# Kernel optimization log

Measured on AMD Instinct MI355X. Metric: run time of the kernel, lower is better.

The kernel has to match this reference:

```python
import jax, jax.numpy as jnp
import numpy as np

NODE_DIM, HIDDEN, PROJ = 5, 128, 256
NUM_MP = 3
BOX = 1.0


def _knn_edges(positions, k, box_length=BOX):
    """Periodic kNN graph. positions: (B,N,3) -> (src, dst) global flat indices, E = B*N*k."""
    B, N, _ = positions.shape

    def per_batch(pos):  # (N,3)
        delta = jnp.abs(pos[:, None, :] - pos[None, :, :])          # (N,N,3)
        delta = jnp.where(delta > 0.5 * box_length, box_length - delta, delta)
        dist = jnp.sqrt(jnp.sum(delta * delta, axis=-1) + 1e-12)    # (N,N)
        _, idx = jax.lax.top_k(-dist, k + 1)                        # k+1 smallest
        return idx[:, 1:]                                           # drop self -> (N,k)

    nbrs = jax.vmap(per_batch)(positions)                           # (B,N,k)
    offset = (jnp.arange(B) * N)[:, None, None]
    src = jnp.broadcast_to(jnp.arange(N)[None, :, None], (B, N, k)) + offset
    dst = nbrs + offset
    return src.reshape(-1), dst.reshape(-1)


def setup_inputs() -> dict:
    key = jax.random.key(0)
    ks = jax.random.split(key, 16)
    B, N = 8, 2048
    s = 0.05
    inp = {
        "x": jax.random.normal(ks[0], (B, N, NODE_DIM), jnp.float32),
        "positions": jax.random.uniform(ks[1], (B, N, 3), jnp.float32),
        "k": 16,
        # encoder: Linear(5,128)+ReLU, Linear(128,128)+ReLU
        "enc_w0": jax.random.normal(ks[2], (NODE_DIM, HIDDEN), jnp.float32) * s,
        "enc_b0": jnp.zeros((HIDDEN,), jnp.float32),
        "enc_w1": jax.random.normal(ks[3], (HIDDEN, HIDDEN), jnp.float32) * s,
        "enc_b1": jnp.zeros((HIDDEN,), jnp.float32),
        # message nets: Linear(2H,H)+ReLU per round
        "msg_w": jax.random.normal(ks[4], (NUM_MP, 2 * HIDDEN, HIDDEN), jnp.float32) * s,
        "msg_b": jnp.zeros((NUM_MP, HIDDEN), jnp.float32),
        # update nets: Linear(2H,H)+ReLU per round
        "upd_w": jax.random.normal(ks[5], (NUM_MP, 2 * HIDDEN, HIDDEN), jnp.float32) * s,
        "upd_b": jnp.zeros((NUM_MP, HIDDEN), jnp.float32),
        # projection head: Linear(H,H)+ReLU, Linear(H,proj)
        "proj_w0": jax.random.normal(ks[6], (HIDDEN, HIDDEN), jnp.float32) * s,
        "proj_b0": jnp.zeros((HIDDEN,), jnp.float32),
        "proj_w1": jax.random.normal(ks[7], (HIDDEN, PROJ), jnp.float32) * s,
        "proj_b1": jnp.zeros((PROJ,), jnp.float32),
    }
    return inp


def reference(x, positions, k, enc_w0, enc_b0, enc_w1, enc_b1,
              msg_w, msg_b, upd_w, upd_b, proj_w0, proj_b0, proj_w1, proj_b1):
    B, N, _ = x.shape
    BN = B * N
    relu = jax.nn.relu

    # encoder over flattened nodes
    h = relu(x.reshape(BN, -1) @ enc_w0 + enc_b0)
    h = relu(h @ enc_w1 + enc_b1)

    src, dst = _knn_edges(positions, k)
    E = src.shape[0]
    deg = jax.ops.segment_sum(jnp.ones((E,), h.dtype), dst, num_segments=BN)
    inv_deg = 1.0 / jnp.clip(deg, 1.0)

    for i in range(NUM_MP):
        # per-edge message: concat(sender, receiver) -> Linear+ReLU
        msg = relu(jnp.concatenate([h[src], h[dst]], axis=-1) @ msg_w[i] + msg_b[i])
        # mean aggregation at destination nodes
        agg = jax.ops.segment_sum(msg, dst, num_segments=BN) * inv_deg[:, None]
        # residual update
        h = h + relu(jnp.concatenate([h, agg], axis=-1) @ upd_w[i] + upd_b[i])

    z = relu(h @ proj_w0 + proj_b0) @ proj_w1 + proj_b1
    return z.reshape(B, N, PROJ), h.reshape(B, N, HIDDEN)
```

## Files before the change

### kernel.cpp

```cpp
#include <hip/hip_runtime.h>
#include <stdint.h>
#include <math.h>

#define NN 2048
#define BB 8
#define BN (BB*NN)
#define KK 16
#define EE (BN*KK)
#define HID 128
#define PROJ_D 256
#define QPB 16

typedef unsigned long long u64;
typedef unsigned short ushort_t;
typedef __attribute__((ext_vector_type(8))) short short8;
typedef __attribute__((ext_vector_type(4))) float f32x4;

__device__ __forceinline__ u64 wave_min_u64(u64 v) {
  #pragma unroll
  for (int off = 32; off > 0; off >>= 1) {
    u64 o = __shfl_xor(v, off);
    v = o < v ? o : v;
  }
  return v;
}

__global__ __launch_bounds__(1024) void knn_kernel(const float* __restrict__ pos,
                                                   int* __restrict__ nbr,
                                                   int* __restrict__ cnt) {
  __shared__ float4 Ps[NN];
  __shared__ unsigned Hist[QPB * 256];
  const int b  = blockIdx.x >> 7;
  const int qb = blockIdx.x & 127;
  const int wave = threadIdx.x >> 6;
  const int lane = threadIdx.x & 63;
  const int i = qb * QPB + wave;
  const float* P = pos + (size_t)b * NN * 3;

  for (int t = threadIdx.x; t < NN; t += 1024)
    Ps[t] = make_float4(P[t*3], P[t*3+1], P[t*3+2], 0.f);
  __syncthreads();

  const float4 pi = Ps[i];
  const float xi = pi.x, yi = pi.y, zi = pi.z;
  unsigned* H = &Hist[wave * 256];

  float d[32];
  #pragma unroll
  for (int t = 0; t < 32; t++) {
    int j = t * 64 + lane;
    float4 pj = Ps[j];
    float ax = fabsf(xi - pj.x), ay = fabsf(yi - pj.y), az = fabsf(zi - pj.z);
    float dx = fminf(ax, 1.0f - ax);
    float dy = fminf(ay, 1.0f - ay);
    float dz = fminf(az, 1.0f - az);
    float s = __fadd_rn(__fadd_rn(__fadd_rn(__fmul_rn(dx,dx), __fmul_rn(dy,dy)),
                                  __fmul_rn(dz,dz)), 1e-12f);
    d[t] = __fsqrt_rn(s);
  }

  float scale = 1024.0f;
  int bstar = 0; unsigned C = 0;
  for (;;) {
    *(uint4*)&H[lane * 4] = make_uint4(0u, 0u, 0u, 0u);
    #pragma unroll
    for (int t = 0; t < 32; t++) {
      int bin = (int)(d[t] * scale);
      if (bin < 256) atomicAdd(&H[bin], 1u);
    }
    uint4 cv = *(const uint4*)&H[lane * 4];
    unsigned s4 = cv.x + cv.y + cv.z + cv.w;
    unsigned incl = s4;
    #pragma unroll
    for (int off = 1; off < 64; off <<= 1) {
      unsigned v = __shfl_up(incl, off);
      if (lane >= off) incl += v;
    }
    unsigned total = __shfl(incl, 63);
    if (total >= 17u) {
      unsigned base = incl - s4;
      bool has = (incl >= 17u) && (base < 17u);
      u64 hmask = __ballot(has);
      int srcl = __ffsll((unsigned long long)hmask) - 1;
      int bl = 0; unsigned Cl = 0;
      if (has) {
        if (base + cv.x >= 17u)                    { bl = lane*4 + 0; Cl = base; }
        else if (base + cv.x + cv.y >= 17u)        { bl = lane*4 + 1; Cl = base + cv.x; }
        else if (base + cv.x + cv.y + cv.z >= 17u) { bl = lane*4 + 2; Cl = base + cv.x + cv.y; }
        else                                       { bl = lane*4 + 3; Cl = base + cv.x + cv.y + cv.z; }
      }
      bstar = __shfl(bl, srcl);
      C     = __shfl(Cl, srcl);
      break;
    }
    scale *= 0.25f;
  }
  const int m = 17 - (int)C;

  u64 lst[6];
  #pragma unroll
  for (int t = 0; t < 6; t++) lst[t] = ~0ull;
  #pragma unroll
  for (int t = 0; t < 32; t++) {
    int bin = (int)(d[t] * scale);
    u64 key = ((u64)__float_as_uint(d[t]) << 11) | (unsigned)(t * 64 + lane);
    u64 cand = (bin == bstar) ? key : ~0ull;
    if (cand < lst[5]) {
      lst[5] = cand;
      #pragma unroll
      for (int u = 5; u > 0; u--) {
        u64 a = lst[u-1], c2 = lst[u];
        lst[u-1] = a < c2 ? a : c2;
        lst[u]   = a < c2 ? c2 : a;
      }
    }
  }

  u64 kstar = 0;
  #pragma unroll 1
  for (int r = 0; r < m; r++) {
    u64 h0 = lst[0];
    u64 gm = wave_min_u64(h0);
    kstar = gm;
    bool win = (h0 == gm);
    #pragma unroll
    for (int u = 0; u < 5; u++) lst[u] = win ? lst[u+1] : lst[u];
    lst[5] = win ? ~0ull : lst[5];
  }

  int* outp = nbr + ((size_t)b * NN + i) * KK;
  int total = 0;
  #pragma unroll
  for (int t = 0; t < 32; t++) {
    int j = t * 64 + lane;
    u64 key = ((u64)__float_as_uint(d[t]) << 11) | (unsigned)j;
    bool pred = (key <= kstar) && (j != i);
    u64 msk = __ballot(pred);
    if (pred) {
      int ofs = total + __popcll(msk & ((1ull << lane) - 1ull));
      outp[ofs] = b * NN + j;
      atomicAdd(&cnt[b * NN + j], 1);
    }
    total += __popcll(msk);
  }
}

__global__ __launch_bounds__(256) void scan_kernel(const int* __restrict__ cnt,
                                                   int* __restrict__ row_ptr) {
  __shared__ int ps[256];
  int t = threadIdx.x;
  const int4* cv = (const int4*)(cnt + t * 64);
  int4 c[16];
  int s = 0;
  #pragma unroll
  for (int i = 0; i < 16; i++) {
    c[i] = cv[i];
    s += c[i].x + c[i].y + c[i].z + c[i].w;
  }
  ps[t] = s;
  __syncthreads();
  for (int off = 1; off < 256; off <<= 1) {
    int v = 0;
    if (t >= off) v = ps[t - off];
    __syncthreads();
    ps[t] += v;
    __syncthreads();
  }
  int run = t ? ps[t - 1] : 0;
  int4* rp = (int4*)(row_ptr + t * 64);
  #pragma unroll
  for (int i = 0; i < 16; i++) {
    int4 o;
    o.x = run; run += c[i].x;
    o.y = run; run += c[i].y;
    o.z = run; run += c[i].z;
    o.w = run; run += c[i].w;
    rp[i] = o;
  }
  if (t == 255) row_ptr[BN] = run;
}

__global__ __launch_bounds__(256) void fill_kernel(const int* __restrict__ nbr,
                                                   const int* __restrict__ row_ptr,
                                                   int* __restrict__ fill,
                                                   int* __restrict__ col) {
  int e = blockIdx.x * 256 + threadIdx.x;
  int d = nbr[e];
  int srcn = e >> 4;
  int p = row_ptr[d] + atomicAdd(&fill[d], 1);
  col[p] = srcn;
}

__global__ __launch_bounds__(256) void enc0_kernel(const float* __restrict__ x,
                                                   const float* __restrict__ w0,
                                                   const float* __restrict__ b0,
                                                   float* __restrict__ h) {
  int t = blockIdx.x * 256 + threadIdx.x;
  int m = t >> 5;
  int c = (t & 31) * 4;
  float xv[5];
  #pragma unroll
  for (int d = 0; d < 5; d++) xv[d] = x[m * 5 + d];
  float4 acc = *(const float4*)&b0[c];
  #pragma unroll
  for (int d = 0; d < 5; d++) {
    float4 w = *(const float4*)&w0[d * HID + c];
    acc.x += xv[d] * w.x; acc.y += xv[d] * w.y;
    acc.z += xv[d] * w.z; acc.w += xv[d] * w.w;
  }
  acc.x = fmaxf(acc.x, 0.f); acc.y = fmaxf(acc.y, 0.f);
  acc.z = fmaxf(acc.z, 0.f); acc.w = fmaxf(acc.w, 0.f);
  *(float4*)&h[(size_t)m * HID + c] = acc;
}


__device__ __forceinline__ ushort_t bf16_rne(float x) {
  unsigned u = __float_as_uint(x);
  unsigned r = u + 0x7FFFu + ((u >> 16) & 1u);
  return (ushort_t)(r >> 16);
}
__device__ __forceinline__ float bf16_to_f(ushort_t h) {
  return __uint_as_float(((unsigned)h) << 16);
}

__device__ __forceinline__ void cvt8(const float4 f0, const float4 f1,
                                     short8& hi, short8& lo) {
  float f[8] = {f0.x, f0.y, f0.z, f0.w, f1.x, f1.y, f1.z, f1.w};
  #pragma unroll
  for (int e = 0; e < 8; e++) {
    ushort_t h = bf16_rne(f[e]);
    ushort_t l = bf16_rne(f[e] - bf16_to_f(h));
    hi[e] = (short)h;
    lo[e] = (short)l;
  }
}

__global__ __launch_bounds__(256) void prep_w_kernel(
    const float* __restrict__ enc_w1, const float* __restrict__ msg_w,
    const float* __restrict__ upd_w, const float* __restrict__ proj_w0,
    const float* __restrict__ proj_w1, ushort_t* __restrict__ wfrag) {
  int u = blockIdx.x >> 3;
  int c = (blockIdx.x & 7) * 256 + threadIdx.x;
  const float* src;
  int ldW = HID;
  if (u == 0) src = enc_w1;
  else if (u <= 6)  { int i = (u-1)>>1; int hf = (u-1)&1; src = msg_w + ((size_t)i*256 + hf*128) * HID; }
  else if (u <= 12) { int i = (u-7)>>1; int hf = (u-7)&1; src = upd_w + ((size_t)i*256 + hf*128) * HID; }
  else if (u == 13) src = proj_w0;
  else { src = proj_w1 + (u - 14) * 128; ldW = PROJ_D; }

  int ks = c >> 9, ct = (c >> 6) & 7, lane = c & 63;
  int colc = ct * 16 + (lane & 15);
  int k0 = ks * 32 + ((lane >> 4) << 3);
  float f[8];
  #pragma unroll
  for (int e = 0; e < 8; e++) f[e] = src[(size_t)(k0 + e) * ldW + colc];
  short8 hv, lv;
  cvt8(make_float4(f[0],f[1],f[2],f[3]), make_float4(f[4],f[5],f[6],f[7]), hv, lv);
  *(short8*)&wfrag[(size_t)u * 32768 + (size_t)c * 8] = hv;
  *(short8*)&wfrag[(size_t)u * 32768 + 16384 + (size_t)c * 8] = lv;
}

__device__ __forceinline__ void stage_A_convert(ushort_t* Ahi, ushort_t* Alo,
                                                const float* A, int m0, int tid) {
  #pragma unroll
  for (int i = 0; i < 4; i++) {
    int c = tid + i * 256;
    int row = c >> 4, kg = c & 15;
    const float4* ap = (const float4*)(A + (((size_t)m0 + row) << 7) + (kg << 3));
    short8 hv, lv;
    cvt8(ap[0], ap[1], hv, lv);
    int idx = (((row >> 4) * 4 + (kg >> 2)) * 64 + ((row & 15) | ((kg & 3) << 4))) * 8;
    *(short8*)&Ahi[idx] = hv;
    *(short8*)&Alo[idx] = lv;
  }
}

__device__ __forceinline__ void unit_mfma(f32x4 acc[8], const ushort_t* wf,
                                          const ushort_t* Ahi, const ushort_t* Alo,
                                          ushort_t* Bhi, ushort_t* Blo,
                                          int tid, int lane, int wid) {
  #pragma unroll 1
  for (int half = 0; half < 2; half++) {
    __syncthreads();
    const short8* ghi = (const short8*)(wf + half * 8192);
    const short8* glo = (const short8*)(wf + 16384 + half * 8192);
    #pragma unroll
    for (int i = 0; i < 4; i++) {
      ((short8*)Bhi)[tid + i * 256] = ghi[tid + i * 256];
      ((short8*)Blo)[tid + i * 256] = glo[tid + i * 256];
    }
    __syncthreads();
    #pragma unroll
    for (int ks2 = 0; ks2 < 2; ks2++) {
      int ksA = half * 2 + ks2;
      short8 ah = *(const short8*)&Ahi[((wid * 4 + ksA) * 64 + lane) * 8];
      short8 al = *(const short8*)&Alo[((wid * 4 + ksA) * 64 + lane) * 8];
      #pragma unroll
      for (int ct = 0; ct < 8; ct++) {
        short8 bh = *(const short8*)&Bhi[((ks2 * 8 + ct) * 64 + lane) * 8];
        short8 bl = *(const short8*)&Blo[((ks2 * 8 + ct) * 64 + lane) * 8];
        acc[ct] = __builtin_amdgcn_mfma_f32_16x16x32_bf16(ah, bh, acc[ct], 0, 0, 0);
        acc[ct] = __builtin_amdgcn_mfma_f32_16x16x32_bf16(ah, bl, acc[ct], 0, 0, 0);
        acc[ct] = __builtin_amdgcn_mfma_f32_16x16x32_bf16(al, bh, acc[ct], 0, 0, 0);
      }
    }
  }
}

__device__ __forceinline__ void unit_mfma_h(f32x4 acc[4], const ushort_t* wf,
                                            int ct0,
                                            const ushort_t* Ahi, const ushort_t* Alo,
                                            ushort_t* Bhi, ushort_t* Blo,
                                            int tid, int lane, int wid) {
  #pragma unroll 1
  for (int half = 0; half < 2; half++) {
    __syncthreads();
    #pragma unroll
    for (int i = 0; i < 2; i++) {
      int sc = tid + i * 256;
      int ks2 = sc >> 8;
      int cts = (sc >> 6) & 3;
      int ln  = sc & 63;
      int c = half * 1024 + ks2 * 512 + (ct0 + cts) * 64 + ln;
      ((short8*)Bhi)[sc] = *(const short8*)&wf[(size_t)c * 8];
      ((short8*)Blo)[sc] = *(const short8*)&wf[16384 + (size_t)c * 8];
    }
    __syncthreads();
    #pragma unroll
    for (int ks2 = 0; ks2 < 2; ks2++) {
      int ksA = half * 2 + ks2;
      short8 ah = *(const short8*)&Ahi[((wid * 4 + ksA) * 64 + lane) * 8];
      short8 al = *(const short8*)&Alo[((wid * 4 + ksA) * 64 + lane) * 8];
      #pragma unroll
      for (int ct = 0; ct < 4; ct++) {
        short8 bh = *(const short8*)&Bhi[((ks2 * 4 + ct) * 64 + lane) * 8];
        short8 bl = *(const short8*)&Blo[((ks2 * 4 + ct) * 64 + lane) * 8];
        acc[ct] = __builtin_amdgcn_mfma_f32_16x16x32_bf16(ah, bh, acc[ct], 0, 0, 0);
        acc[ct] = __builtin_amdgcn_mfma_f32_16x16x32_bf16(ah, bl, acc[ct], 0, 0, 0);
        acc[ct] = __builtin_amdgcn_mfma_f32_16x16x32_bf16(al, bh, acc[ct], 0, 0, 0);
      }
    }
  }
}

template<int RELU>
__global__ __launch_bounds__(256, 4) void g1_kernel(
    const float* __restrict__ A, const ushort_t* __restrict__ wf,
    const float* __restrict__ bias, float* __restrict__ out) {
  __shared__ ushort_t Ahi[8192], Alo[8192], Bhi[4096], Blo[4096];
  const int tid = threadIdx.x, lane = tid & 63, wid = tid >> 6;
  const int m0 = blockIdx.x * 64, ct0 = blockIdx.y * 4;
  stage_A_convert(Ahi, Alo, A, m0, tid);
  f32x4 acc[4];
  f32x4 z = {0.f, 0.f, 0.f, 0.f};
  #pragma unroll
  for (int ct = 0; ct < 4; ct++) acc[ct] = z;
  unit_mfma_h(acc, wf, ct0, Ahi, Alo, Bhi, Blo, tid, lane, wid);

  const int rbase = m0 + wid * 16 + ((lane >> 4) << 2);
  const int cb = lane & 15;
  #pragma unroll
  for (int ct = 0; ct < 4; ct++) {
    int n = (ct0 + ct) * 16 + cb;
    float bv = bias ? bias[n] : 0.f;
    #pragma unroll
    for (int r = 0; r < 4; r++) {
      float v = acc[ct][r] + bv;
      if (RELU) v = fmaxf(v, 0.f);
      out[(size_t)(rbase + r) * HID + n] = v;
    }
  }
}

__global__ __launch_bounds__(256, 4) void msg_kernel(
    const float* __restrict__ h, const ushort_t* __restrict__ wfT,
    const ushort_t* __restrict__ wfB, const float* __restrict__ mb,
    float* __restrict__ bufA, float* __restrict__ bufB) {
  __shared__ ushort_t Ahi[8192], Alo[8192], Bhi[8192], Blo[8192];
  const int tid = threadIdx.x, lane = tid & 63, wid = tid >> 6;
  const int m0 = blockIdx.x * 64;
  const int y = blockIdx.y;
  stage_A_convert(Ahi, Alo, h, m0, tid);
  f32x4 acc[8];
  f32x4 z = {0.f, 0.f, 0.f, 0.f};
  #pragma unroll
  for (int ct = 0; ct < 8; ct++) acc[ct] = z;
  unit_mfma(acc, y ? wfB : wfT, Ahi, Alo, Bhi, Blo, tid, lane, wid);

  float* out = y ? bufB : bufA;
  const float* bias = y ? mb : nullptr;
  const int rbase = m0 + wid * 16 + ((lane >> 4) << 2);
  const int cb = lane & 15;
  #pragma unroll
  for (int ct = 0; ct < 8; ct++) {
    int n = ct * 16 + cb;
    float bv = bias ? bias[n] : 0.f;
    #pragma unroll
    for (int r = 0; r < 4; r++)
      out[(size_t)(rbase + r) * HID + n] = acc[ct][r] + bv;
  }
}

__global__ __launch_bounds__(256, 4) void upd_kernel(
    const float* __restrict__ h, const ushort_t* __restrict__ wuT,
    const float* __restrict__ aggF, const ushort_t* __restrict__ wuB,
    const float* __restrict__ ub, float* __restrict__ out) {
  __shared__ ushort_t Ahi[8192], Alo[8192], Bhi[4096], Blo[4096];
  const int tid = threadIdx.x, lane = tid & 63, wid = tid >> 6;
  const int m0 = blockIdx.x * 64, ct0 = blockIdx.y * 4;
  stage_A_convert(Ahi, Alo, h, m0, tid);
  f32x4 acc[4];
  f32x4 z = {0.f, 0.f, 0.f, 0.f};
  #pragma unroll
  for (int ct = 0; ct < 4; ct++) acc[ct] = z;
  unit_mfma_h(acc, wuT, ct0, Ahi, Alo, Bhi, Blo, tid, lane, wid);
  __syncthreads();
  stage_A_convert(Ahi, Alo, aggF, m0, tid);
  unit_mfma_h(acc, wuB, ct0, Ahi, Alo, Bhi, Blo, tid, lane, wid);

  const int rbase = m0 + wid * 16 + ((lane >> 4) << 2);
  const int cb = lane & 15;
  #pragma unroll
  for (int ct = 0; ct < 4; ct++) {
    int n = (ct0 + ct) * 16 + cb;
    float bv = ub[n];
    #pragma unroll
    for (int r = 0; r < 4; r++) {
      float v = fmaxf(acc[ct][r] + bv, 0.f)
              + h[(size_t)(rbase + r) * HID + n];
      out[(size_t)(rbase + r) * HID + n] = v;
    }
  }
}

__global__ __launch_bounds__(256, 4) void proj1_kernel(
    const float* __restrict__ A, const ushort_t* __restrict__ wf01,
    const float* __restrict__ pb1, float* __restrict__ zout) {
  __shared__ ushort_t Ahi[8192], Alo[8192], Bhi[8192], Blo[8192];
  const int tid = threadIdx.x, lane = tid & 63, wid = tid >> 6;
  const int m0 = blockIdx.x * 64;
  const int y = blockIdx.y;
  stage_A_convert(Ahi, Alo, A, m0, tid);
  f32x4 acc[8];
  f32x4 z = {0.f, 0.f, 0.f, 0.f};
  #pragma unroll
  for (int ct = 0; ct < 8; ct++) acc[ct] = z;
  unit_mfma(acc, wf01 + (size_t)y * 32768, Ahi, Alo, Bhi, Blo, tid, lane, wid);

  const int rbase = m0 + wid * 16 + ((lane >> 4) << 2);
  const int cb = lane & 15;
  #pragma unroll
  for (int ct = 0; ct < 8; ct++) {
    int n = y * 128 + ct * 16 + cb;
    float bv = pb1[n];
    #pragma unroll
    for (int r = 0; r < 4; r++)
      zout[(size_t)(rbase + r) * PROJ_D + n] = acc[ct][r] + bv;
  }
}

__global__ __launch_bounds__(256) void agg_kernel(const float* __restrict__ Abuf,
                                                  const float* __restrict__ Bbuf,
                                                  const int* __restrict__ row_ptr,
                                                  const int* __restrict__ col,
                                                  float* __restrict__ agg) {
  int j = blockIdx.x * 2 + (threadIdx.x >> 7);
  int c = threadIdx.x & 127;
  float bj = Bbuf[(size_t)j * HID + c];
  int s = row_ptr[j], e = row_ptr[j + 1];
  float acc = 0.f;
  int p = s;
  for (; p + 4 <= e; p += 4) {
    int i0 = col[p], i1 = col[p+1], i2 = col[p+2], i3 = col[p+3];
    float v0 = Abuf[(size_t)i0 * HID + c];
    float v1 = Abuf[(size_t)i1 * HID + c];
    float v2 = Abuf[(size_t)i2 * HID + c];
    float v3 = Abuf[(size_t)i3 * HID + c];
    acc += fmaxf(v0 + bj, 0.f) + fmaxf(v1 + bj, 0.f)
         + fmaxf(v2 + bj, 0.f) + fmaxf(v3 + bj, 0.f);
  }
  for (; p < e; p++) {
    int i = col[p];
    acc += fmaxf(Abuf[(size_t)i * HID + c] + bj, 0.f);
  }
  float deg = (float)(e - s);
  float inv = 1.0f / fmaxf(deg, 1.0f);
  agg[(size_t)j * HID + c] = acc * inv;
}

extern "C" void kernel_launch(void* const* d_in, const int* in_sizes, int n_in,
                              void* d_out, int out_size, void* d_ws, size_t ws_size,
                              hipStream_t stream) {
  (void)in_sizes; (void)n_in; (void)out_size; (void)ws_size;
  const float* x       = (const float*)d_in[0];
  const float* pos     = (const float*)d_in[1];
  const float* enc_w0  = (const float*)d_in[3];
  const float* enc_b0  = (const float*)d_in[4];
  const float* enc_w1  = (const float*)d_in[5];
  const float* enc_b1  = (const float*)d_in[6];
  const float* msg_w   = (const float*)d_in[7];
  const float* msg_b   = (const float*)d_in[8];
  const float* upd_w   = (const float*)d_in[9];
  const float* upd_b   = (const float*)d_in[10];
  const float* proj_w0 = (const float*)d_in[11];
  const float* proj_b0 = (const float*)d_in[12];
  const float* proj_w1 = (const float*)d_in[13];
  const float* proj_b1 = (const float*)d_in[14];

  char* ws = (char*)d_ws;
  size_t off = 0;
  auto alloc = [&](size_t bytes) -> void* {
    void* p = ws + off;
    off += (bytes + 255) & ~(size_t)255;
    return p;
  };
  int*      nbr     = (int*)alloc((size_t)EE * 4);
  int*      cnt     = (int*)alloc((size_t)BN * 4);
  int*      fill    = (int*)alloc((size_t)BN * 4);
  int*      row_ptr = (int*)alloc((size_t)(BN + 1) * 4);
  int*      col     = (int*)alloc((size_t)EE * 4);
  float*    h_a     = (float*)alloc((size_t)BN * HID * 4);
  float*    h_b     = (float*)alloc((size_t)BN * HID * 4);
  float*    bufA    = (float*)alloc((size_t)BN * HID * 4);
  float*    bufB    = (float*)alloc((size_t)BN * HID * 4);
  float*    bufAgg  = (float*)alloc((size_t)BN * HID * 4);
  ushort_t* wfrag   = (ushort_t*)alloc((size_t)16 * 32768 * 2);
  float*    out     = (float*)d_out;
  float*    hOut    = out + (size_t)BN * PROJ_D;

  hipMemsetAsync(cnt, 0, (size_t)BN * 4 * 2, stream);

  prep_w_kernel<<<128, 256, 0, stream>>>(enc_w1, msg_w, upd_w, proj_w0, proj_w1, wfrag);
  knn_kernel<<<BN / QPB, 1024, 0, stream>>>(pos, nbr, cnt);
  scan_kernel<<<1, 256, 0, stream>>>(cnt, row_ptr);
  fill_kernel<<<EE / 256, 256, 0, stream>>>(nbr, row_ptr, fill, col);

  enc0_kernel<<<BN * 32 / 256, 256, 0, stream>>>(x, enc_w0, enc_b0, bufA);
  g1_kernel<1><<<dim3(BN / 64, 2), 256, 0, stream>>>(bufA, wfrag + 0 * 32768,
                                                     enc_b1, h_a);

  float* hc = h_a;
  float* hn = h_b;
  for (int i = 0; i < 3; i++) {
    msg_kernel<<<dim3(BN / 64, 2), 256, 0, stream>>>(
        hc, wfrag + (size_t)(1 + 2 * i) * 32768,
        wfrag + (size_t)(2 + 2 * i) * 32768, msg_b + (size_t)i * HID,
        bufA, bufB);
    agg_kernel<<<BN / 2, 256, 0, stream>>>(bufA, bufB, row_ptr, col, bufAgg);
    float* target = (i == 2) ? hOut : hn;
    upd_kernel<<<dim3(BN / 64, 2), 256, 0, stream>>>(
        hc, wfrag + (size_t)(7 + 2 * i) * 32768, bufAgg,
        wfrag + (size_t)(8 + 2 * i) * 32768, upd_b + (size_t)i * HID, target);
    hn = hc; hc = target;
  }

  g1_kernel<1><<<dim3(BN / 64, 2), 256, 0, stream>>>(hc, wfrag + 13 * 32768,
                                                     proj_b0, bufA);
  proj1_kernel<<<dim3(BN / 64, 2), 256, 0, stream>>>(
      bufA, wfrag + 14 * 32768, proj_b1, out);
}
```

Before: 241.9 us.

## Fuse neighbor aggregation into update GEMM kernel, staging agg directly in LDS

Removes the separate agg_kernel and the bufAgg intermediate. Each update block now gathers and averages the ReLU'd messages for its 64 rows, converts them to hi/lo bf16 fragments straight into shared memory, and runs both halves of the update GEMM over all 128 output columns. This avoids a full global write and read of the aggregate plus one launch per round. In exchange the grid shrinks from 512 to 256 blocks, each block holds larger LDS tiles, and the gather is done once per row rather than split across column tiles.

```diff
diff --git a/kernel.cpp b/kernel.cpp
--- a/kernel.cpp
+++ b/kernel.cpp
@@ -402,28 +402,79 @@
   }
 }
 
-__global__ __launch_bounds__(256, 4) void upd_kernel(
+__global__ __launch_bounds__(256, 2) void upd_fused_kernel(
     const float* __restrict__ h, const ushort_t* __restrict__ wuT,
-    const float* __restrict__ aggF, const ushort_t* __restrict__ wuB,
-    const float* __restrict__ ub, float* __restrict__ out) {
-  __shared__ ushort_t Ahi[8192], Alo[8192], Bhi[4096], Blo[4096];
+    const ushort_t* __restrict__ wuB, const float* __restrict__ ub,
+    const float* __restrict__ bufA, const float* __restrict__ bufB,
+    const int* __restrict__ row_ptr, const int* __restrict__ col,
+    float* __restrict__ out) {
+  __shared__ ushort_t Ahi[8192], Alo[8192], Bhi[8192], Blo[8192];
   const int tid = threadIdx.x, lane = tid & 63, wid = tid >> 6;
-  const int m0 = blockIdx.x * 64, ct0 = blockIdx.y * 4;
+  const int m0 = blockIdx.x * 64;
+
+  #pragma unroll 1
+  for (int i = 0; i < 4; i++) {
+    int c = tid + i * 256;
+    int row = c >> 4, kg = c & 15;
+    int j = m0 + row;
+    const float4* bjp = (const float4*)(bufB + ((size_t)j << 7) + (kg << 3));
+    float4 bj0 = bjp[0], bj1 = bjp[1];
+    int s = row_ptr[j], e = row_ptr[j + 1];
+    float4 a0 = make_float4(0.f, 0.f, 0.f, 0.f);
+    float4 a1 = make_float4(0.f, 0.f, 0.f, 0.f);
+    int p = s;
+    for (; p + 2 <= e; p += 2) {
+      int j0 = col[p], j1 = col[p + 1];
+      const float4* v0 = (const float4*)(bufA + ((size_t)j0 << 7) + (kg << 3));
+      const float4* v1 = (const float4*)(bufA + ((size_t)j1 << 7) + (kg << 3));
+      float4 x0 = v0[0], x1 = v0[1], y0 = v1[0], y1 = v1[1];
+      a0.x += fmaxf(x0.x + bj0.x, 0.f) + fmaxf(y0.x + bj0.x, 0.f);
+      a0.y += fmaxf(x0.y + bj0.y, 0.f) + fmaxf(y0.y + bj0.y, 0.f);
+      a0.z += fmaxf(x0.z + bj0.z, 0.f) + fmaxf(y0.z + bj0.z, 0.f);
+      a0.w += fmaxf(x0.w + bj0.w, 0.f) + fmaxf(y0.w + bj0.w, 0.f);
+      a1.x += fmaxf(x1.x + bj1.x, 0.f) + fmaxf(y1.x + bj1.x, 0.f);
+      a1.y += fmaxf(x1.y + bj1.y, 0.f) + fmaxf(y1.y + bj1.y, 0.f);
+      a1.z += fmaxf(x1.z + bj1.z, 0.f) + fmaxf(y1.z + bj1.z, 0.f);
+      a1.w += fmaxf(x1.w + bj1.w, 0.f) + fmaxf(y1.w + bj1.w, 0.f);
+    }
+    for (; p < e; p++) {
+      int j0 = col[p];
+      const float4* v0 = (const float4*)(bufA + ((size_t)j0 << 7) + (kg << 3));
+      float4 x0 = v0[0], x1 = v0[1];
+      a0.x += fmaxf(x0.x + bj0.x, 0.f);
+      a0.y += fmaxf(x0.y + bj0.y, 0.f);
+      a0.z += fmaxf(x0.z + bj0.z, 0.f);
+      a0.w += fmaxf(x0.w + bj0.w, 0.f);
+      a1.x += fmaxf(x1.x + bj1.x, 0.f);
+      a1.y += fmaxf(x1.y + bj1.y, 0.f);
+      a1.z += fmaxf(x1.z + bj1.z, 0.f);
+      a1.w += fmaxf(x1.w + bj1.w, 0.f);
+    }
+    float inv = 1.0f / fmaxf((float)(e - s), 1.0f);
+    a0.x *= inv; a0.y *= inv; a0.z *= inv; a0.w *= inv;
+    a1.x *= inv; a1.y *= inv; a1.z *= inv; a1.w *= inv;
+    short8 hv, lv;
+    cvt8(a0, a1, hv, lv);
+    int idx = (((row >> 4) * 4 + (kg >> 2)) * 64 + ((row & 15) | ((kg & 3) << 4))) * 8;
+    *(short8*)&Ahi[idx] = hv;
+    *(short8*)&Alo[idx] = lv;
+  }
+
+  f32x4 acc[8];
+  f32x4 z = {0.f, 0.f, 0.f, 0.f};
+  #pragma unroll
+  for (int ct = 0; ct < 8; ct++) acc[ct] = z;
+  unit_mfma(acc, wuB, Ahi, Alo, Bhi, Blo, tid, lane, wid);
+
+  __syncthreads();
   stage_A_convert(Ahi, Alo, h, m0, tid);
-  f32x4 acc[4];
-  f32x4 z = {0.f, 0.f, 0.f, 0.f};
-  #pragma unroll
-  for (int ct = 0; ct < 4; ct++) acc[ct] = z;
-  unit_mfma_h(acc, wuT, ct0, Ahi, Alo, Bhi, Blo, tid, lane, wid);
-  __syncthreads();
-  stage_A_convert(Ahi, Alo, aggF, m0, tid);
-  unit_mfma_h(acc, wuB, ct0, Ahi, Alo, Bhi, Blo, tid, lane, wid);
+  unit_mfma(acc, wuT, Ahi, Alo, Bhi, Blo, tid, lane, wid);
 
   const int rbase = m0 + wid * 16 + ((lane >> 4) << 2);
   const int cb = lane & 15;
   #pragma unroll
-  for (int ct = 0; ct < 4; ct++) {
-    int n = (ct0 + ct) * 16 + cb;
+  for (int ct = 0; ct < 8; ct++) {
+    int n = ct * 16 + cb;
     float bv = ub[n];
     #pragma unroll
     for (int r = 0; r < 4; r++) {
@@ -458,35 +509,6 @@
     for (int r = 0; r < 4; r++)
       zout[(size_t)(rbase + r) * PROJ_D + n] = acc[ct][r] + bv;
   }
-}
-
-__global__ __launch_bounds__(256) void agg_kernel(const float* __restrict__ Abuf,
-                                                  const float* __restrict__ Bbuf,
-                                                  const int* __restrict__ row_ptr,
-                                                  const int* __restrict__ col,
-                                                  float* __restrict__ agg) {
-  int j = blockIdx.x * 2 + (threadIdx.x >> 7);
-  int c = threadIdx.x & 127;
-  float bj = Bbuf[(size_t)j * HID + c];
-  int s = row_ptr[j], e = row_ptr[j + 1];
-  float acc = 0.f;
-  int p = s;
-  for (; p + 4 <= e; p += 4) {
-    int i0 = col[p], i1 = col[p+1], i2 = col[p+2], i3 = col[p+3];
-    float v0 = Abuf[(size_t)i0 * HID + c];
-    float v1 = Abuf[(size_t)i1 * HID + c];
-    float v2 = Abuf[(size_t)i2 * HID + c];
-    float v3 = Abuf[(size_t)i3 * HID + c];
-    acc += fmaxf(v0 + bj, 0.f) + fmaxf(v1 + bj, 0.f)
-         + fmaxf(v2 + bj, 0.f) + fmaxf(v3 + bj, 0.f);
-  }
-  for (; p < e; p++) {
-    int i = col[p];
-    acc += fmaxf(Abuf[(size_t)i * HID + c] + bj, 0.f);
-  }
-  float deg = (float)(e - s);
-  float inv = 1.0f / fmaxf(deg, 1.0f);
-  agg[(size_t)j * HID + c] = acc * inv;
 }
 
 extern "C" void kernel_launch(void* const* d_in, const int* in_sizes, int n_in,
@@ -524,7 +546,6 @@
   float*    h_b     = (float*)alloc((size_t)BN * HID * 4);
   float*    bufA    = (float*)alloc((size_t)BN * HID * 4);
   float*    bufB    = (float*)alloc((size_t)BN * HID * 4);
-  float*    bufAgg  = (float*)alloc((size_t)BN * HID * 4);
   ushort_t* wfrag   = (ushort_t*)alloc((size_t)16 * 32768 * 2);
   float*    out     = (float*)d_out;
   float*    hOut    = out + (size_t)BN * PROJ_D;
@@ -547,11 +568,11 @@
         hc, wfrag + (size_t)(1 + 2 * i) * 32768,
         wfrag + (size_t)(2 + 2 * i) * 32768, msg_b + (size_t)i * HID,
         bufA, bufB);
-    agg_kernel<<<BN / 2, 256, 0, stream>>>(bufA, bufB, row_ptr, col, bufAgg);
     float* target = (i == 2) ? hOut : hn;
-    upd_kernel<<<dim3(BN / 64, 2), 256, 0, stream>>>(
-        hc, wfrag + (size_t)(7 + 2 * i) * 32768, bufAgg,
-        wfrag + (size_t)(8 + 2 * i) * 32768, upd_b + (size_t)i * HID, target);
+    upd_fused_kernel<<<BN / 64, 256, 0, stream>>>(
+        hc, wfrag + (size_t)(7 + 2 * i) * 32768,
+        wfrag + (size_t)(8 + 2 * i) * 32768, upd_b + (size_t)i * HID,
+        bufA, bufB, row_ptr, col, target);
     hn = hc; hc = target;
   }
 
```

After: 276.0 us. 1.14x slower.
